# Optimization experiments

Measured on AMD Instinct MI355X. Metric: run time of the kernel, lower is better.

Reference implementation:

```python
import jax, jax.numpy as jnp
import numpy as np

B, S, F = 256, 192, 64
HD, L, PRED = 1024, 2, 48


def setup_inputs() -> dict:
    key = jax.random.key(0)
    ks = jax.random.split(key, 9)
    s_in = 1.0 / np.sqrt(F)
    s_h = 1.0 / np.sqrt(HD)
    return {
        "x": jax.random.normal(ks[0], (B, S, F), dtype=jnp.float32),
        "W_hidden": jax.random.uniform(ks[1], (F, HD), jnp.float32, -s_in, s_in),
        "b_hidden": jax.random.uniform(ks[2], (HD,), jnp.float32, -s_in, s_in),
        "Wih": jax.random.uniform(ks[3], (L, HD, HD), jnp.float32, -s_h, s_h),
        "Whh": jax.random.uniform(ks[4], (L, HD, HD), jnp.float32, -s_h, s_h),
        "bih": jax.random.uniform(ks[5], (L, HD), jnp.float32, -s_h, s_h),
        "bhh": jax.random.uniform(ks[6], (L, HD), jnp.float32, -s_h, s_h),
        "Wo": jax.random.uniform(ks[7], (HD, F), jnp.float32, -s_h, s_h),
        "bo": jax.random.uniform(ks[8], (F,), jnp.float32, -s_h, s_h),
    }


def reference(x, W_hidden, b_hidden, Wih, Whh, bih, bhh, Wo, bo):
    # x: [B, S, F]
    x_concat = x @ W_hidden + b_hidden          # [B, S, HD]
    xs = jnp.swapaxes(x_concat, 0, 1)           # [S, B, HD] for time scan
    h0 = jnp.zeros((L, x.shape[0], HD), x.dtype)

    def step(h, x_t):
        # h: [L, B, HD], x_t: [B, HD]; standard tanh-RNN stacked layers
        inp = x_t
        new_h = []
        for l in range(L):
            hl = jnp.tanh(inp @ Wih[l] + bih[l] + h[l] @ Whh[l] + bhh[l])
            new_h.append(hl)
            inp = hl
        h_new = jnp.stack(new_h)
        return h_new, h_new[-1]

    _, ys = jax.lax.scan(step, h0, xs)           # ys: [S, B, HD] top-layer states
    # torch code stores h for t in [0, S-2] only (drops last timestep)
    H = jnp.swapaxes(ys[:-1], 0, 1)              # [B, S-1, HD]
    H = jax.nn.relu(H)
    out = H @ Wo + bo                            # [B, S-1, F]
    return out[:, -PRED:, :]
```

## Files before the change

kernel.cpp:

```cpp
#include <hip/hip_runtime.h>
#include <hip/hip_bf16.h>

#define B    256
#define S    192
#define F    64
#define HD   1024
#define PRED 48
#define TSTART (S - 1 - PRED)
#define NSLOT 48

typedef __attribute__((ext_vector_type(8))) short short8;
typedef __attribute__((ext_vector_type(4))) float f32x4;
typedef unsigned int u32;

static __device__ __forceinline__ short f2bf(float f) {
    __hip_bfloat16 h = __float2bfloat16(f);
    return *reinterpret_cast<short*>(&h);
}
static __device__ __forceinline__ f32x4 mfma16(short8 a, short8 b, f32x4 c) {
    return __builtin_amdgcn_mfma_f32_16x16x32_bf16(a, b, c, 0, 0, 0);
}
static __device__ __forceinline__ short8 ld8(const short* p) {
    return *reinterpret_cast<const short8*>(p);
}
static __device__ __forceinline__ void st_state(short* p, short v) {
    __hip_atomic_store(p, v, __ATOMIC_RELAXED, __HIP_MEMORY_SCOPE_AGENT);
}
static __device__ __forceinline__ u32 ld_flag(const u32* p) {
    return __hip_atomic_load(p, __ATOMIC_RELAXED, __HIP_MEMORY_SCOPE_AGENT);
}
static __device__ __forceinline__ void st_flag(u32* p, u32 v) {
    __hip_atomic_store(p, v, __ATOMIC_RELAXED, __HIP_MEMORY_SCOPE_AGENT);
}

__global__ void fold_kernel(const float* __restrict__ Wh,
                            const float* __restrict__ Wih0,
                            float* __restrict__ Wfold) {
    const int n = (blockIdx.x & 3) * 256 + threadIdx.x;
    const int f = blockIdx.x >> 2;
    float a = 0.f;
#pragma unroll 16
    for (int k = 0; k < HD; ++k)
        a += Wh[f * HD + k] * Wih0[(size_t)k * HD + n];
    Wfold[f * HD + n] = a;
}

__global__ void bias_kernel(const float* __restrict__ bh,
                            const float* __restrict__ Wih0,
                            const float* __restrict__ bih,
                            const float* __restrict__ bhh,
                            float* __restrict__ bf0,
                            float* __restrict__ bf1) {
    __shared__ float red[256];
    const int nl = threadIdx.x & 15;
    const int kc = threadIdx.x >> 4;
    const int n  = blockIdx.x * 16 + nl;
    float a = 0.f;
#pragma unroll 8
    for (int k = kc * 64; k < kc * 64 + 64; ++k)
        a += bh[k] * Wih0[(size_t)k * HD + n];
    red[threadIdx.x] = a;
    __syncthreads();
    if (kc == 0) {
        float s = 0.f;
#pragma unroll
        for (int j = 0; j < 16; ++j) s += red[j * 16 + nl];
        bf0[n] = s + bih[n] + bhh[n];
        bf1[n] = bih[HD + n] + bhh[HD + n];
    }
}

__global__ void transpose_cast(const float* __restrict__ src,
                               short* __restrict__ dst, int K, int N) {
    __shared__ float tile[64][65];
    const int nk = K >> 6;
    const int bk = blockIdx.x % nk;
    const int bn = blockIdx.x / nk;
    const int i  = threadIdx.x;
    {
        const int c4 = (i & 15) * 4;
        for (int it = 0; it < 4; ++it) {
            const int k = (i >> 4) + it * 16;
            const float4 v = *reinterpret_cast<const float4*>(
                &src[(size_t)(bk * 64 + k) * N + bn * 64 + c4]);
            tile[k][c4 + 0] = v.x; tile[k][c4 + 1] = v.y;
            tile[k][c4 + 2] = v.z; tile[k][c4 + 3] = v.w;
        }
    }
    __syncthreads();
    {
        const int n  = i >> 2;
        const int kb = (i & 3) * 16;
        short* dp = &dst[(size_t)(bn * 64 + n) * K + bk * 64 + kb];
#pragma unroll
        for (int j = 0; j < 16; ++j) dp[j] = f2bf(tile[kb + j][n]);
    }
}

__global__ void xcast(const float* __restrict__ x, short* __restrict__ xb) {
    const size_t i = ((size_t)blockIdx.x * 256 + threadIdx.x) * 4;
    const float4 v = *reinterpret_cast<const float4*>(&x[i]);
    short4 o;
    o.x = f2bf(v.x); o.y = f2bf(v.y); o.z = f2bf(v.z); o.w = f2bf(v.w);
    *reinterpret_cast<short4*>(&xb[i]) = o;
}

static __device__ __forceinline__ void stage1(char* lds, const short* __restrict__ src,
                                              int row0) {
    const int tid = threadIdx.x;
#pragma unroll
    for (int it = 0; it < 8; ++it) {
        const int idx = it * 512 + tid;
        const int r   = (idx >> 2) & 31;
        const int off = ((idx >> 7) << 6) + ((idx & 3) << 4);
        const f32x4 v = *reinterpret_cast<const f32x4*>(
            (const char*)src + (size_t)(row0 + r) * 2048 + off);
        *reinterpret_cast<f32x4*>(lds + (idx << 4)) = v;
    }
}

static __device__ __forceinline__ void pre_load(f32x4 (&pre)[8],
                                                const short* __restrict__ src,
                                                int row0) {
    const int tid = threadIdx.x;
#pragma unroll
    for (int it = 0; it < 8; ++it) {
        const int idx = it * 512 + tid;
        const int r   = (idx >> 2) & 31;
        const int off = ((idx >> 7) << 6) + ((idx & 3) << 4);
        pre[it] = *reinterpret_cast<const f32x4*>(
            (const char*)src + (size_t)(row0 + r) * 2048 + off);
    }
}
static __device__ __forceinline__ void pre_write(char* lds, const f32x4 (&pre)[8]) {
    const int tid = threadIdx.x;
#pragma unroll
    for (int it = 0; it < 8; ++it) {
        const int idx = it * 512 + tid;
        *reinterpret_cast<f32x4*>(lds + (idx << 4)) = pre[it];
    }
}

static __device__ __forceinline__ f32x4 gemmLG(const char* ldsA,
                                               const short* __restrict__ bp,
                                               f32x4 acc_in) {
    f32x4 acc0 = acc_in, acc1 = {0.f,0.f,0.f,0.f};
    short8 b0[8], b1[8];
#pragma unroll
    for (int j = 0; j < 8; ++j) b0[j] = ld8(bp + j * 32);
#pragma unroll
    for (int c = 0; c < 4; ++c) {
        if (c < 3) {
            short8* nxt = (c & 1) ? b0 : b1;
#pragma unroll
            for (int j = 0; j < 8; ++j) nxt[j] = ld8(bp + (c + 1) * 256 + j * 32);
        }
        const short8* cur = (c & 1) ? b1 : b0;
#pragma unroll
        for (int j = 0; j < 8; ++j) {
            const short8 a = *reinterpret_cast<const short8*>(
                ldsA + (c * 8 + j) * 2048);
            if (j & 1) acc1 = mfma16(a, cur[j], acc1);
            else       acc0 = mfma16(a, cur[j], acc0);
        }
    }
    return acc0 + acc1;
}

__global__ __launch_bounds__(512, 1) void rnn_pers(
    const short* __restrict__ xbf,
    const short* __restrict__ WfoldT, const float* __restrict__ bf0,
    const short* __restrict__ WhhT0, const short* __restrict__ WihT1,
    const short* __restrict__ WhhT1, const float* __restrict__ bf1,
    short* h0h, short* h1h, u32* flags0, u32* flags1) {

    extern __shared__ char lds[];

    const int bid   = blockIdx.x;
    const int xcd   = bid & 7;
    const int u     = bid >> 3;
    const int layer = u & 1;
    const int rt    = ((xcd & 3) << 1) | ((u >> 1) & 1);
    const int ct    = ((xcd >> 2) << 3) | ((u >> 2) & 7);
    const int w     = threadIdx.x >> 6;
    const int mh    = w & 1;
    const int nq    = w >> 1;
    const int l     = threadIdx.x & 63;
    const int lr    = l & 15, kg = l >> 4;
    const int row0  = rt * 32;
    const int m0    = row0 + mh * 16;
    const int n0    = ct * 64 + nq * 16;
    const int col   = n0 + lr;
    const int rb    = m0 + kg * 4;
    const char* ldsA = lds + mh * 1024 + lr * 64 + kg * 16;

    const float bb = (layer ? bf1 : bf0)[col];
    u32* myflag = (layer ? flags1 : flags0) + (rt * 16 + ct) * 32;
    const int tid = threadIdx.x;

    if (layer == 0) {
        const short* wf = WfoldT + (size_t)col * F + kg * 8;
        const short8 wf0 = ld8(wf), wf1 = ld8(wf + 32);
        const short* whh0p = WhhT0 + (size_t)col * HD + kg * 8;
        for (int k = 0; k < S - 1; ++k) {
            const short* xp = xbf + ((size_t)(m0 + lr) * S + k) * F + kg * 8;
            const short8 xa0 = ld8(xp);
            const short8 xa1 = ld8(xp + 32);
            if (k > 0) {
                __syncthreads();
                if (tid < 16) {
                    const u32* f = flags0 + (rt * 16 + tid) * 32;
                    while (ld_flag(f) < (u32)k) __builtin_amdgcn_s_sleep(1);
                } else if (tid < 32 && k >= 46) {
                    const u32* f = flags1 + (rt * 16 + (tid - 16)) * 32;
                    while (ld_flag(f) < (u32)(k - 45)) __builtin_amdgcn_s_sleep(1);
                }
                __syncthreads();
                stage1(lds, h0h + (size_t)((k - 1) % NSLOT) * B * HD, row0);
                __syncthreads();
            }
            f32x4 acc = {0.f, 0.f, 0.f, 0.f};
            acc = mfma16(xa0, wf0, acc);
            acc = mfma16(xa1, wf1, acc);
            if (k > 0) acc = gemmLG(ldsA, whh0p, acc);
            short* hd = h0h + (size_t)(k % NSLOT) * B * HD;
#pragma unroll
            for (int r = 0; r < 4; ++r)
                st_state(&hd[(size_t)(rb + r) * HD + col],
                         f2bf(tanhf(acc[r] + bb)));
            __syncthreads();
            if (tid == 0) st_flag(myflag, (u32)(k + 1));
        }
    } else {
        if (tid == 0) st_flag(myflag, 1u);
        char* ldsBbuf = lds + 65536;
        const char* ldsB = ldsBbuf + mh * 1024 + lr * 64 + kg * 16;
        const short* wih1p = WihT1 + (size_t)col * HD + kg * 8;
        const short* whh1p = WhhT1 + (size_t)col * HD + kg * 8;

        if (tid < 16) {
            const u32* f = flags0 + (rt * 16 + tid) * 32;
            while (ld_flag(f) < 1u) __builtin_amdgcn_s_sleep(1);
        }
        __syncthreads();
        stage1(lds, h0h, row0);
        __syncthreads();

        for (int k = 1; k < S; ++k) {
            const int t = k - 1;
            f32x4 acc = {0.f, 0.f, 0.f, 0.f};
            acc = gemmLG(ldsA, wih1p, acc);
            if (tid < 16) {
                if (k + 1 < S) {
                    const u32* f = flags0 + (rt * 16 + tid) * 32;
                    while (ld_flag(f) < (u32)(k + 1)) __builtin_amdgcn_s_sleep(1);
                }
            } else if (tid < 32 && t > 0) {
                const u32* f = flags1 + (rt * 16 + (tid - 16)) * 32;
                while (ld_flag(f) < (u32)k) __builtin_amdgcn_s_sleep(1);
            }
            __syncthreads();
            f32x4 pre[8];
            if (k + 1 < S)
                pre_load(pre, h0h + (size_t)(k % NSLOT) * B * HD, row0);
            if (t > 0) {
                stage1(ldsBbuf, h1h + (size_t)((t - 1) % NSLOT) * B * HD, row0);
                __syncthreads();
                acc = gemmLG(ldsB, whh1p, acc);
            }
#pragma unroll
            for (int r = 0; r < 4; ++r)
                st_state(&h1h[(size_t)(t % NSLOT) * B * HD
                              + (size_t)(rb + r) * HD + col],
                         f2bf(tanhf(acc[r] + bb)));
            __syncthreads();
            if (tid == 0) st_flag(myflag, (u32)(k + 1));
            if (k + 1 < S) {
                pre_write(lds, pre);
                __syncthreads();
            }
        }
    }
}

__global__ __launch_bounds__(256) void outgemm(
    const short* __restrict__ h1h, const short* __restrict__ WoT,
    const float* __restrict__ bo, float* __restrict__ out) {
    const int w = threadIdx.x >> 6, l = threadIdx.x & 63;
    const int lr = l & 15, kg = l >> 4;
    const int m0 = blockIdx.x * 64 + w * 16;
    const int arow = m0 + lr;
    const u32 bidx = (u32)arow / 48u;
    const u32 p    = (u32)arow % 48u;
    const u32 slot = (143u + p) % 48u;

    f32x4 acc[4] = {{0.f,0.f,0.f,0.f},{0.f,0.f,0.f,0.f},
                    {0.f,0.f,0.f,0.f},{0.f,0.f,0.f,0.f}};
    const short* ap = h1h + ((size_t)slot * B + bidx) * HD + kg * 8;
    const short* bp = WoT + (size_t)lr * HD + kg * 8;
#pragma unroll 4
    for (int k0 = 0; k0 < HD; k0 += 32) {
        short8 a = ld8(ap + k0);
#pragma unroll
        for (int j = 0; j < 8; ++j) a[j] = (a[j] < 0) ? (short)0 : a[j];
#pragma unroll
        for (int c = 0; c < 4; ++c)
            acc[c] = mfma16(a, ld8(bp + (size_t)c * 16 * HD + k0), acc[c]);
    }
    const int rb = m0 + kg * 4;
#pragma unroll
    for (int c = 0; c < 4; ++c) {
        const float bbv = bo[c * 16 + lr];
#pragma unroll
        for (int r = 0; r < 4; ++r)
            out[(size_t)(rb + r) * F + c * 16 + lr] = acc[c][r] + bbv;
    }
}

extern "C" void kernel_launch(void* const* d_in, const int* in_sizes, int n_in,
                              void* d_out, int out_size, void* d_ws, size_t ws_size,
                              hipStream_t stream) {
    const float* x   = (const float*)d_in[0];
    const float* Wh  = (const float*)d_in[1];
    const float* bh  = (const float*)d_in[2];
    const float* Wih = (const float*)d_in[3];
    const float* Whh = (const float*)d_in[4];
    const float* bih = (const float*)d_in[5];
    const float* bhh = (const float*)d_in[6];
    const float* Wo  = (const float*)d_in[7];
    const float* bo  = (const float*)d_in[8];
    float* out = (float*)d_out;

    char* p = (char*)d_ws;
    float* Wfold  = (float*)p; p += (size_t)F * HD * 4;
    float* bf0    = (float*)p; p += HD * 4;
    float* bf1    = (float*)p; p += HD * 4;
    short* WfoldT = (short*)p; p += (size_t)HD * F * 2;
    short* WhhT0  = (short*)p; p += (size_t)HD * HD * 2;
    short* WihT1  = (short*)p; p += (size_t)HD * HD * 2;
    short* WhhT1  = (short*)p; p += (size_t)HD * HD * 2;
    short* WoT    = (short*)p; p += (size_t)F * HD * 2;
    short* h0h    = (short*)p; p += (size_t)NSLOT * B * HD * 2;
    short* h1h    = (short*)p; p += (size_t)NSLOT * B * HD * 2;
    short* xbf    = (short*)p; p += (size_t)B * S * F * 2;
    u32*   sync   = (u32*)p;  p += 65536;

    hipMemsetAsync(sync, 0, 65536, stream);

    fold_kernel<<<256, 256, 0, stream>>>(Wh, Wih, Wfold);
    bias_kernel<<<64, 256, 0, stream>>>(bh, Wih, bih, bhh, bf0, bf1);
    transpose_cast<<<16, 256, 0, stream>>>(Wfold, WfoldT, F, HD);
    transpose_cast<<<256, 256, 0, stream>>>(Whh, WhhT0, HD, HD);
    transpose_cast<<<256, 256, 0, stream>>>(Wih + (size_t)HD * HD, WihT1, HD, HD);
    transpose_cast<<<256, 256, 0, stream>>>(Whh + (size_t)HD * HD, WhhT1, HD, HD);
    transpose_cast<<<16, 256, 0, stream>>>(Wo, WoT, HD, F);
    xcast<<<(B * S * F) / (256 * 4), 256, 0, stream>>>(x, xbf);

    u32* flags0 = sync;
    u32* flags1 = sync + 4096;
    void* args[] = {
        (void*)&xbf, (void*)&WfoldT, (void*)&bf0, (void*)&WhhT0,
        (void*)&WihT1, (void*)&WhhT1, (void*)&bf1,
        (void*)&h0h, (void*)&h1h, (void*)&flags0, (void*)&flags1
    };
    hipLaunchCooperativeKernel((void*)rnn_pers, dim3(256), dim3(512),
                               args, 131072, stream);

    outgemm<<<192, 256, 0, stream>>>(h1h, WoT, bo, out);
}
```

Baseline: 2.175 ms.

## Split layer-1 blocks into Wih and Whh halves with split staging flags

Layer-1 blocks now split their 8 waves into two halves. One half computes the input-projection GEMM on h0 while the other computes the recurrent GEMM on h1, and the partial sums are combined through LDS. Staging of h0 and h1 into LDS is also split between the halves. Separate 'stored' and 'gathered' flags replace the single layer-1 flag, so layer-0 buffer reuse is gated on the gather completing rather than the store. Layer-0 now waits for flags and stages at the end of each step instead of the start. This aims to shorten the layer-1 critical path per timestep, at the cost of more LDS (139 KB), an extra barrier and more flag traffic.

```diff
diff --git a/kernel.cpp b/kernel.cpp
--- a/kernel.cpp
+++ b/kernel.cpp
@@ -8,6 +8,7 @@
 #define PRED 48
 #define TSTART (S - 1 - PRED)
 #define NSLOT 48
+#define BHD  ((size_t)B * HD)
 
 typedef __attribute__((ext_vector_type(8))) short short8;
 typedef __attribute__((ext_vector_type(4))) float f32x4;
@@ -105,7 +106,7 @@
     *reinterpret_cast<short4*>(&xb[i]) = o;
 }
 
-static __device__ __forceinline__ void stage1(char* lds, const short* __restrict__ src,
+static __device__ __forceinline__ void stage8(char* lds, const short* __restrict__ src,
                                               int row0) {
     const int tid = threadIdx.x;
 #pragma unroll
@@ -118,26 +119,16 @@
         *reinterpret_cast<f32x4*>(lds + (idx << 4)) = v;
     }
 }
-
-static __device__ __forceinline__ void pre_load(f32x4 (&pre)[8],
-                                                const short* __restrict__ src,
-                                                int row0) {
-    const int tid = threadIdx.x;
-#pragma unroll
-    for (int it = 0; it < 8; ++it) {
-        const int idx = it * 512 + tid;
+static __device__ __forceinline__ void stage16(char* lds, const short* __restrict__ src,
+                                               int row0, int g) {
+#pragma unroll
+    for (int it = 0; it < 16; ++it) {
+        const int idx = it * 256 + g;
         const int r   = (idx >> 2) & 31;
         const int off = ((idx >> 7) << 6) + ((idx & 3) << 4);
-        pre[it] = *reinterpret_cast<const f32x4*>(
+        const f32x4 v = *reinterpret_cast<const f32x4*>(
             (const char*)src + (size_t)(row0 + r) * 2048 + off);
-    }
-}
-static __device__ __forceinline__ void pre_write(char* lds, const f32x4 (&pre)[8]) {
-    const int tid = threadIdx.x;
-#pragma unroll
-    for (int it = 0; it < 8; ++it) {
-        const int idx = it * 512 + tid;
-        *reinterpret_cast<f32x4*>(lds + (idx << 4)) = pre[it];
+        *reinterpret_cast<f32x4*>(lds + (idx << 4)) = v;
     }
 }
 
@@ -167,12 +158,37 @@
     return acc0 + acc1;
 }
 
+static __device__ __forceinline__ void gemm2x(const char* lA0, const char* lA1,
+                                              const short* __restrict__ bp,
+                                              f32x4& accLo, f32x4& accHi) {
+    short8 b0[8], b1[8];
+#pragma unroll
+    for (int j = 0; j < 8; ++j) b0[j] = ld8(bp + j * 32);
+#pragma unroll
+    for (int c = 0; c < 4; ++c) {
+        if (c < 3) {
+            short8* nxt = (c & 1) ? b0 : b1;
+#pragma unroll
+            for (int j = 0; j < 8; ++j) nxt[j] = ld8(bp + (c + 1) * 256 + j * 32);
+        }
+        const short8* cur = (c & 1) ? b1 : b0;
+#pragma unroll
+        for (int j = 0; j < 8; ++j) {
+            const int ch = c * 8 + j;
+            accLo = mfma16(*reinterpret_cast<const short8*>(lA0 + ch * 2048),
+                           cur[j], accLo);
+            accHi = mfma16(*reinterpret_cast<const short8*>(lA1 + ch * 2048),
+                           cur[j], accHi);
+        }
+    }
+}
+
 __global__ __launch_bounds__(512, 1) void rnn_pers(
     const short* __restrict__ xbf,
     const short* __restrict__ WfoldT, const float* __restrict__ bf0,
     const short* __restrict__ WhhT0, const short* __restrict__ WihT1,
     const short* __restrict__ WhhT1, const float* __restrict__ bf1,
-    short* h0h, short* h1h, u32* flags0, u32* flags1) {
+    short* h0h, short* h1h, u32* flags0, u32* flags1S, u32* flags1G) {
 
     extern __shared__ char lds[];
 
@@ -183,101 +199,119 @@
     const int rt    = ((xcd & 3) << 1) | ((u >> 1) & 1);
     const int ct    = ((xcd >> 2) << 3) | ((u >> 2) & 7);
     const int w     = threadIdx.x >> 6;
-    const int mh    = w & 1;
-    const int nq    = w >> 1;
     const int l     = threadIdx.x & 63;
     const int lr    = l & 15, kg = l >> 4;
     const int row0  = rt * 32;
-    const int m0    = row0 + mh * 16;
-    const int n0    = ct * 64 + nq * 16;
-    const int col   = n0 + lr;
-    const int rb    = m0 + kg * 4;
-    const char* ldsA = lds + mh * 1024 + lr * 64 + kg * 16;
-
-    const float bb = (layer ? bf1 : bf0)[col];
-    u32* myflag = (layer ? flags1 : flags0) + (rt * 16 + ct) * 32;
-    const int tid = threadIdx.x;
+    const int tid   = threadIdx.x;
 
     if (layer == 0) {
+        const int mh = w & 1, nq = w >> 1;
+        const int m0 = row0 + mh * 16;
+        const int col = ct * 64 + nq * 16 + lr;
+        const int rb  = m0 + kg * 4;
+        const char* ldsA = lds + mh * 1024 + lr * 64 + kg * 16;
+        const float bb = bf0[col];
+        u32* myflag = flags0 + (rt * 16 + ct) * 32;
         const short* wf = WfoldT + (size_t)col * F + kg * 8;
         const short8 wf0 = ld8(wf), wf1 = ld8(wf + 32);
         const short* whh0p = WhhT0 + (size_t)col * HD + kg * 8;
+
         for (int k = 0; k < S - 1; ++k) {
             const short* xp = xbf + ((size_t)(m0 + lr) * S + k) * F + kg * 8;
-            const short8 xa0 = ld8(xp);
-            const short8 xa1 = ld8(xp + 32);
-            if (k > 0) {
-                __syncthreads();
-                if (tid < 16) {
-                    const u32* f = flags0 + (rt * 16 + tid) * 32;
-                    while (ld_flag(f) < (u32)k) __builtin_amdgcn_s_sleep(1);
-                } else if (tid < 32 && k >= 46) {
-                    const u32* f = flags1 + (rt * 16 + (tid - 16)) * 32;
-                    while (ld_flag(f) < (u32)(k - 45)) __builtin_amdgcn_s_sleep(1);
-                }
-                __syncthreads();
-                stage1(lds, h0h + (size_t)((k - 1) % NSLOT) * B * HD, row0);
-                __syncthreads();
-            }
             f32x4 acc = {0.f, 0.f, 0.f, 0.f};
-            acc = mfma16(xa0, wf0, acc);
-            acc = mfma16(xa1, wf1, acc);
+            acc = mfma16(ld8(xp),      wf0, acc);
+            acc = mfma16(ld8(xp + 32), wf1, acc);
             if (k > 0) acc = gemmLG(ldsA, whh0p, acc);
-            short* hd = h0h + (size_t)(k % NSLOT) * B * HD;
+            short* hd = h0h + (size_t)(k % NSLOT) * BHD;
 #pragma unroll
             for (int r = 0; r < 4; ++r)
                 st_state(&hd[(size_t)(rb + r) * HD + col],
                          f2bf(tanhf(acc[r] + bb)));
             __syncthreads();
             if (tid == 0) st_flag(myflag, (u32)(k + 1));
+            if (k + 1 < S - 1) {
+                if (tid < 16) {
+                    const u32* f = flags0 + (rt * 16 + tid) * 32;
+                    while (ld_flag(f) < (u32)(k + 1)) __builtin_amdgcn_s_sleep(1);
+                } else if (tid >= 64 && tid < 80 && (k + 1) >= 48) {
+                    const u32* f = flags1G + (rt * 16 + (tid - 64)) * 32;
+                    while (ld_flag(f) < (u32)(k + 1 - 47)) __builtin_amdgcn_s_sleep(1);
+                }
+                __syncthreads();
+                stage8(lds, h0h + (size_t)(k % NSLOT) * BHD, row0);
+                __syncthreads();
+            }
         }
     } else {
-        if (tid == 0) st_flag(myflag, 1u);
-        char* ldsBbuf = lds + 65536;
-        const char* ldsB = ldsBbuf + mh * 1024 + lr * 64 + kg * 16;
+        char*  ldsB = lds + 65536;
+        float* ldsP = reinterpret_cast<float*>(lds + 131072);
+        const int half = w >> 2;
+        const int wq   = w & 3;
+        const int g256 = tid & 255;
+        const int col  = ct * 64 + wq * 16 + lr;
+        const char* lA0 = lds  + lr * 64 + kg * 16;
+        const char* lA1 = lds  + 1024 + lr * 64 + kg * 16;
+        const char* lB0 = ldsB + lr * 64 + kg * 16;
+        const char* lB1 = ldsB + 1024 + lr * 64 + kg * 16;
         const short* wih1p = WihT1 + (size_t)col * HD + kg * 8;
         const short* whh1p = WhhT1 + (size_t)col * HD + kg * 8;
-
+        const float bb = bf1[col];
+        u32* myflagS = flags1S + (rt * 16 + ct) * 32;
+        u32* myflagG = flags1G + (rt * 16 + ct) * 32;
+
+        if (tid == 0) st_flag(myflagS, 1u);
         if (tid < 16) {
             const u32* f = flags0 + (rt * 16 + tid) * 32;
             while (ld_flag(f) < 1u) __builtin_amdgcn_s_sleep(1);
         }
         __syncthreads();
-        stage1(lds, h0h, row0);
+        stage8(lds, h0h, row0);
         __syncthreads();
+        if (tid == 0) st_flag(myflagG, 1u);
 
         for (int k = 1; k < S; ++k) {
             const int t = k - 1;
-            f32x4 acc = {0.f, 0.f, 0.f, 0.f};
-            acc = gemmLG(ldsA, wih1p, acc);
-            if (tid < 16) {
-                if (k + 1 < S) {
+            f32x4 aLo = {0.f,0.f,0.f,0.f}, aHi = {0.f,0.f,0.f,0.f};
+            if (half == 0) {
+                gemm2x(lA0, lA1, wih1p, aLo, aHi);
+#pragma unroll
+                for (int r = 0; r < 4; ++r) {
+                    ldsP[(kg * 4 + r) * 64 + wq * 16 + lr]        = aLo[r];
+                    ldsP[(16 + kg * 4 + r) * 64 + wq * 16 + lr]   = aHi[r];
+                }
+            } else if (t > 0) {
+                gemm2x(lB0, lB1, whh1p, aLo, aHi);
+            }
+            __syncthreads();
+            if (half == 1) {
+                short* hd = h1h + (size_t)(t % NSLOT) * BHD;
+#pragma unroll
+                for (int r = 0; r < 4; ++r) {
+                    const float vLo = tanhf(aLo[r] + bb
+                        + ldsP[(kg * 4 + r) * 64 + wq * 16 + lr]);
+                    const float vHi = tanhf(aHi[r] + bb
+                        + ldsP[(16 + kg * 4 + r) * 64 + wq * 16 + lr]);
+                    st_state(&hd[(size_t)(row0 + kg * 4 + r) * HD + col], f2bf(vLo));
+                    st_state(&hd[(size_t)(row0 + 16 + kg * 4 + r) * HD + col], f2bf(vHi));
+                }
+            }
+            __syncthreads();
+            if (tid == 0) st_flag(myflagS, (u32)(k + 1));
+            if (k + 1 < S) {
+                if (tid < 16) {
                     const u32* f = flags0 + (rt * 16 + tid) * 32;
                     while (ld_flag(f) < (u32)(k + 1)) __builtin_amdgcn_s_sleep(1);
+                } else if (tid >= 64 && tid < 80) {
+                    const u32* f = flags1S + (rt * 16 + (tid - 64)) * 32;
+                    while (ld_flag(f) < (u32)(k + 1)) __builtin_amdgcn_s_sleep(1);
                 }
-            } else if (tid < 32 && t > 0) {
-                const u32* f = flags1 + (rt * 16 + (tid - 16)) * 32;
-                while (ld_flag(f) < (u32)k) __builtin_amdgcn_s_sleep(1);
-            }
-            __syncthreads();
-            f32x4 pre[8];
-            if (k + 1 < S)
-                pre_load(pre, h0h + (size_t)(k % NSLOT) * B * HD, row0);
-            if (t > 0) {
-                stage1(ldsBbuf, h1h + (size_t)((t - 1) % NSLOT) * B * HD, row0);
                 __syncthreads();
-                acc = gemmLG(ldsB, whh1p, acc);
-            }
-#pragma unroll
-            for (int r = 0; r < 4; ++r)
-                st_state(&h1h[(size_t)(t % NSLOT) * B * HD
-                              + (size_t)(rb + r) * HD + col],
-                         f2bf(tanhf(acc[r] + bb)));
-            __syncthreads();
-            if (tid == 0) st_flag(myflag, (u32)(k + 1));
-            if (k + 1 < S) {
-                pre_write(lds, pre);
+                if (half == 0)
+                    stage16(lds,  h0h + (size_t)(k % NSLOT) * BHD, row0, g256);
+                else
+                    stage16(ldsB, h1h + (size_t)((k - 1) % NSLOT) * BHD, row0, g256);
                 __syncthreads();
+                if (tid == 0) st_flag(myflagG, (u32)(k + 1));
             }
         }
     }
@@ -356,15 +390,17 @@
     transpose_cast<<<16, 256, 0, stream>>>(Wo, WoT, HD, F);
     xcast<<<(B * S * F) / (256 * 4), 256, 0, stream>>>(x, xbf);
 
-    u32* flags0 = sync;
-    u32* flags1 = sync + 4096;
+    u32* flags0  = sync;
+    u32* flags1S = sync + 4096;
+    u32* flags1G = sync + 8192;
     void* args[] = {
         (void*)&xbf, (void*)&WfoldT, (void*)&bf0, (void*)&WhhT0,
         (void*)&WihT1, (void*)&WhhT1, (void*)&bf1,
-        (void*)&h0h, (void*)&h1h, (void*)&flags0, (void*)&flags1
+        (void*)&h0h, (void*)&h1h,
+        (void*)&flags0, (void*)&flags1S, (void*)&flags1G
     };
     hipLaunchCooperativeKernel((void*)rnn_pers, dim3(256), dim3(512),
-                               args, 131072, stream);
+                               args, 139264, stream);
 
     outgemm<<<192, 256, 0, stream>>>(h1h, WoT, bo, out);
 }
```

Result: no change. 2.171 ms (-0.2%).
